# Performance work log

Measured on AMD Instinct MI355X. Metric: run time of the kernel, lower is better.

## Reference

```python
import jax, jax.numpy as jnp
import numpy as np

N_NODES = 10000
N_EDGES = 160000
IN_DIM = 512
HID = 256
HEADS = 4
OUT_DIM = 512
NEG_SLOPE = 0.2  # PyG GATConv default


def _glorot(key, shape):
    fan_in, fan_out = shape[0], shape[-1]
    lim = jnp.sqrt(6.0 / (fan_in + fan_out))
    return jax.random.uniform(key, shape, jnp.float32, -lim, lim)


def setup_inputs() -> dict:
    key = jax.random.key(0)
    ks = jax.random.split(key, 16)
    x = jax.random.normal(ks[0], (N_NODES, IN_DIM), jnp.float32)
    edge_index = jax.random.randint(ks[1], (2, N_EDGES), 0, N_NODES, jnp.int64)
    # layer 1: GATConv(512 -> 256, heads=4, concat) -> out 1024
    W1 = _glorot(ks[2], (IN_DIM, HEADS * HID))
    att_src1 = _glorot(ks[3], (HEADS, HID))
    att_dst1 = _glorot(ks[4], (HEADS, HID))
    b1 = jnp.zeros((HEADS * HID,), jnp.float32)
    # layer 2: GATConv(1024 -> 256, heads=4, concat) -> out 1024
    W2 = _glorot(ks[5], (HEADS * HID, HEADS * HID))
    att_src2 = _glorot(ks[6], (HEADS, HID))
    att_dst2 = _glorot(ks[7], (HEADS, HID))
    b2 = jnp.zeros((HEADS * HID,), jnp.float32)
    # final fc: 1024 -> 512
    fcW = _glorot(ks[8], (HEADS * HID, OUT_DIM))
    fcb = jnp.zeros((OUT_DIM,), jnp.float32)
    return dict(x=x, edge_index=edge_index, W1=W1, att_src1=att_src1,
                att_dst1=att_dst1, b1=b1, W2=W2, att_src2=att_src2,
                att_dst2=att_dst2, b2=b2, fcW=fcW, fcb=fcb)


def gat_conv(x, src, dst, W, att_src, att_dst, bias):
    # x: [N, F_in]; src/dst: [E] (self-loops already included)
    N = x.shape[0]
    h = (x @ W).reshape(N, HEADS, HID)                       # [N, H, C]
    a_src = jnp.sum(h * att_src, axis=-1)                    # [N, H]
    a_dst = jnp.sum(h * att_dst, axis=-1)                    # [N, H]
    e = jax.nn.leaky_relu(a_src[src] + a_dst[dst], NEG_SLOPE)  # [E, H]
    # numerically stable segment softmax over destination nodes
    m = jax.ops.segment_max(e, dst, num_segments=N)          # [N, H]
    e = jnp.exp(e - m[dst])
    s = jax.ops.segment_sum(e, dst, num_segments=N)          # [N, H]
    alpha = e / (s[dst] + 1e-16)                             # [E, H]
    msg = alpha[:, :, None] * h[src]                         # [E, H, C]
    out = jax.ops.segment_sum(msg, dst, num_segments=N)      # [N, H, C]
    return out.reshape(N, HEADS * HID) + bias


def reference(x, edge_index, W1, att_src1, att_dst1, b1,
              W2, att_src2, att_dst2, b2, fcW, fcb):
    N = x.shape[0]
    loops = jnp.arange(N, dtype=edge_index.dtype)
    src = jnp.concatenate([edge_index[0], loops])  # PyG add_self_loops=True
    dst = jnp.concatenate([edge_index[1], loops])
    h = gat_conv(x, src, dst, W1, att_src1, att_dst1, b1)
    h = jax.nn.relu(h)  # dropout is identity in eval mode
    h = gat_conv(h, src, dst, W2, att_src2, att_dst2, b2)
    h = jax.nn.relu(h)
    return h @ fcW + fcb
```

## Files before the change

kernel.cpp:

```cpp
#include <hip/hip_runtime.h>
#include <hip/hip_bf16.h>

#define NN 10000
#define NE 160000
#define NET 170000
#define IN_DIM 512
#define D1 1024
#define HEADS 4
#define HID 256
#define OUT_DIM 512
#define NEG_SLOPE 0.2f

typedef __attribute__((ext_vector_type(8))) short bf16x8;
typedef __attribute__((ext_vector_type(4))) float f32x4;

__device__ inline float b2f(unsigned short b) {
    union { unsigned u; float f; } x; x.u = ((unsigned)b) << 16; return x.f;
}
__device__ inline unsigned short f2b(float f) {
    union { float f; unsigned u; } x; x.f = f;
    unsigned u = x.u;
    unsigned r = u + 0x7FFFu + ((u >> 16) & 1u);
    return (unsigned short)(r >> 16);
}
__device__ inline float lrelu(float v) { return v > 0.f ? v : NEG_SLOPE * v; }

__device__ inline void load_edge(const void* ei, int f64, int e, int& s, int& d) {
    if (f64) {
        const long long* p = (const long long*)ei;
        s = (int)p[e]; d = (int)p[NE + e];
    } else {
        const int* p = (const int*)ei;
        s = p[e]; d = p[NE + e];
    }
}

__global__ void count_kernel(const void* ei, const int* flag, int* counts) {
    int e = blockIdx.x * blockDim.x + threadIdx.x;
    if (e >= NET) return;
    int s, d;
    if (e < NE) load_edge(ei, *flag, e, s, d);
    else d = e - NE;
    atomicAdd(&counts[d], 1);
}

__global__ __launch_bounds__(256) void scan_kernel(const int* counts, int* indptr) {
    __shared__ int part[256];
    int t = threadIdx.x;
    int base = t * 40;
    int local[40];
    int sum = 0;
#pragma unroll
    for (int k = 0; k < 40; k++) {
        int i = base + k;
        int c = (i < NN) ? counts[i] : 0;
        local[k] = sum;
        sum += c;
    }
    part[t] = sum;
    __syncthreads();
    for (int off = 1; off < 256; off <<= 1) {
        int v = (t >= off) ? part[t - off] : 0;
        __syncthreads();
        part[t] += v;
        __syncthreads();
    }
    int excl = part[t] - sum;
#pragma unroll
    for (int k = 0; k < 40; k++) {
        int i = base + k;
        if (i < NN) indptr[i] = excl + local[k];
    }
    if (t == 255) indptr[NN] = part[255];
}

__global__ void fill_kernel(const void* ei, const int* flag, const int* indptr,
                            int* cursor, int* csr_src) {
    int e = blockIdx.x * blockDim.x + threadIdx.x;
    if (e >= NET) return;
    int s, d;
    if (e < NE) load_edge(ei, *flag, e, s, d);
    else { s = e - NE; d = s; }
    int pos = indptr[d] + atomicAdd(&cursor[d], 1);
    csr_src[pos] = s;
}

__device__ void tpose_tile(const float* __restrict__ in, unsigned short* __restrict__ out,
                           int R, int C, int bx, int by) {
    __shared__ float tile[32][33];
    int tx = threadIdx.x & 31, ty = threadIdx.x >> 5;
    int c = bx * 32 + tx;
#pragma unroll
    for (int r0 = 0; r0 < 32; r0 += 8) {
        int r = by * 32 + ty + r0;
        tile[ty + r0][tx] = in[(size_t)r * C + c];
    }
    __syncthreads();
    int oc = by * 32 + tx;
#pragma unroll
    for (int r0 = 0; r0 < 32; r0 += 8) {
        int orow = bx * 32 + ty + r0;
        out[(size_t)orow * R + oc] = f2b(tile[tx][ty + r0]);
    }
}

#define INIT_NB 40
#define CVT_NB 5000
#define TP1_NB 512
#define TP2_NB 1024
#define TP3_NB 512
__global__ __launch_bounds__(256) void setup_kernel(
    const int* ei32, int* flag, int* counts, int* cursor,
    const float* __restrict__ x, unsigned short* __restrict__ xb,
    const float* __restrict__ W1, unsigned short* __restrict__ W1t,
    const float* __restrict__ W2, unsigned short* __restrict__ W2t,
    const float* __restrict__ fcW, unsigned short* __restrict__ fcWt) {
    int b = blockIdx.x;
    if (b < INIT_NB) {
        int i = b * 256 + threadIdx.x;
        if (i < NN) { counts[i] = 0; cursor[i] = 0; }
        if (b == 0) {
            __shared__ int nz;
            if (threadIdx.x == 0) nz = 0;
            __syncthreads();
            int acc = 0;
            for (int k = threadIdx.x; k < 500; k += 256) acc |= ei32[2 * k + 1];
            if (acc) atomicOr(&nz, 1);
            __syncthreads();
            if (threadIdx.x == 0) flag[0] = (nz == 0) ? 1 : 0;
        }
        return;
    }
    b -= INIT_NB;
    if (b < CVT_NB) {
        int i = b * 256 + threadIdx.x;
        float4 v = reinterpret_cast<const float4*>(x)[i];
        ushort4 o;
        o.x = f2b(v.x); o.y = f2b(v.y); o.z = f2b(v.z); o.w = f2b(v.w);
        reinterpret_cast<ushort4*>(xb)[i] = o;
        return;
    }
    b -= CVT_NB;
    if (b < TP1_NB) { tpose_tile(W1, W1t, IN_DIM, D1, b & 31, b >> 5); return; }
    b -= TP1_NB;
    if (b < TP2_NB) { tpose_tile(W2, W2t, D1, D1, b & 31, b >> 5); return; }
    b -= TP2_NB;
    tpose_tile(fcW, fcWt, D1, OUT_DIM, b & 15, b >> 4);
}

template<int TBM, int TBN>
__global__ __launch_bounds__(256) void gemmT(
    const unsigned short* __restrict__ A, const unsigned short* __restrict__ B,
    const float* __restrict__ bias, float* __restrict__ Cf, unsigned short* __restrict__ Cb,
    int M, int N, int K, int NB) {
    constexpr int FM = TBM / 32;
    constexpr int FN = TBN / 32;
    constexpr int AISS = TBM / 32;
    constexpr int BISS = TBN / 32;
    constexpr int ABUF = TBM * 64;
    constexpr int BBUF = TBN * 64;
    __shared__ __align__(16) unsigned short As[2 * ABUF];
    __shared__ __align__(16) unsigned short Bs[2 * BBUF];
    int t = threadIdx.x;
    int nwg = gridDim.x;
    int q = nwg >> 3, r = nwg & 7;
    int xcd = blockIdx.x & 7, jj = blockIdx.x >> 3;
    int wg = (xcd < r ? xcd * (q + 1) : r * (q + 1) + (xcd - r) * q) + jj;
    int row0 = (wg / NB) * TBM, col0 = (wg % NB) * TBN;

    int w = t >> 6, l = t & 63;
    int wr = w >> 1, wc = w & 1;
    f32x4 acc[FM][FN] = {};

    int srow = w * 8 + (l >> 3);
    int scs = ((l & 7) ^ (l >> 3)) * 8;
    const unsigned short* ap[AISS];
    const unsigned short* bp[BISS];
#pragma unroll
    for (int i = 0; i < AISS; i++)
        ap[i] = A + (size_t)min(row0 + i * 32 + srow, M - 1) * K + scs;
#pragma unroll
    for (int i = 0; i < BISS; i++)
        bp[i] = B + (size_t)(col0 + i * 32 + srow) * K + scs;

    int rr = l & 15;
    int rb = (rr & 7) << 4;
    int kb0 = (l >> 4) << 4;
    int c_l = l & 15, r_h = (l >> 4) * 4;

#define GLD(src, dst) __builtin_amdgcn_global_load_lds( \
        (const __attribute__((address_space(1))) void*)(src), \
        (__attribute__((address_space(3))) void*)(dst), 16, 0, 0)

#pragma unroll
    for (int i = 0; i < AISS; i++) { GLD(ap[i], As + i * 2048 + w * 512); ap[i] += 64; }
#pragma unroll
    for (int i = 0; i < BISS; i++) { GLD(bp[i], Bs + i * 2048 + w * 512); bp[i] += 64; }
    __syncthreads();

    int cur = 0;
    for (int k0 = 0; k0 < K; k0 += 64) {
        int nxt = cur ^ 1;
        if (k0 + 64 < K) {
#pragma unroll
            for (int i = 0; i < AISS; i++) {
                GLD(ap[i], As + nxt * ABUF + i * 2048 + w * 512);
                ap[i] += 64;
            }
#pragma unroll
            for (int i = 0; i < BISS; i++) {
                GLD(bp[i], Bs + nxt * BBUF + i * 2048 + w * 512);
                bp[i] += 64;
            }
        }
        const char* Ab = (const char*)(As + cur * ABUF);
        const char* Bb = (const char*)(Bs + cur * BBUF);
#pragma unroll
        for (int ks = 0; ks < 2; ks++) {
            int kb = ((ks << 6) | kb0) ^ rb;
            bf16x8 af[FM], bfv[FN];
#pragma unroll
            for (int mi = 0; mi < FM; mi++)
                af[mi] = *reinterpret_cast<const bf16x8*>(
                    Ab + (wr * (TBM / 2) + mi * 16 + rr) * 128 + kb);
#pragma unroll
            for (int ni = 0; ni < FN; ni++)
                bfv[ni] = *reinterpret_cast<const bf16x8*>(
                    Bb + (wc * (TBN / 2) + ni * 16 + rr) * 128 + kb);
#pragma unroll
            for (int mi = 0; mi < FM; mi++)
#pragma unroll
                for (int ni = 0; ni < FN; ni++)
                    acc[mi][ni] = __builtin_amdgcn_mfma_f32_16x16x32_bf16(
                        af[mi], bfv[ni], acc[mi][ni], 0, 0, 0);
        }
        __syncthreads();
        cur = nxt;
    }
#undef GLD

#pragma unroll
    for (int mi = 0; mi < FM; mi++)
#pragma unroll
        for (int ni = 0; ni < FN; ni++) {
            int gc = col0 + wc * (TBN / 2) + ni * 16 + c_l;
#pragma unroll
            for (int j = 0; j < 4; j++) {
                int gr = row0 + wr * (TBM / 2) + mi * 16 + r_h + j;
                if (gr < M) {
                    float v = acc[mi][ni][j];
                    if (bias) v += bias[gc];
                    if (Cf) Cf[(size_t)gr * N + gc] = v;
                    if (Cb) Cb[(size_t)gr * N + gc] = f2b(v);
                }
            }
        }
}

__global__ __launch_bounds__(256) void att_kernel(const unsigned short* __restrict__ hb,
                                                  const float* __restrict__ att_s,
                                                  const float* __restrict__ att_d,
                                                  float* __restrict__ aS, float* __restrict__ aD) {
    int node = blockIdx.x * 4 + (threadIdx.x >> 6);
    int l = threadIdx.x & 63;
    int head = l >> 4, qq = l & 15;
    const unsigned short* hrow = hb + (size_t)node * D1 + head * HID + qq * 16;
    bf16x8 h0 = *reinterpret_cast<const bf16x8*>(hrow);
    bf16x8 h1 = *reinterpret_cast<const bf16x8*>(hrow + 8);
    const float* asp = att_s + head * HID + qq * 16;
    const float* adp = att_d + head * HID + qq * 16;
    float ps = 0.f, pd = 0.f;
#pragma unroll
    for (int c = 0; c < 8; c++) {
        float hv = b2f((unsigned short)h0[c]);
        float hw = b2f((unsigned short)h1[c]);
        ps += hv * asp[c] + hw * asp[8 + c];
        pd += hv * adp[c] + hw * adp[8 + c];
    }
#pragma unroll
    for (int off = 1; off <= 8; off <<= 1) {
        ps += __shfl_xor(ps, off);
        pd += __shfl_xor(pd, off);
    }
    if (qq == 0) {
        aS[node * HEADS + head] = ps;
        aD[node * HEADS + head] = pd;
    }
}

__global__ __launch_bounds__(256) void agg_kernel(const unsigned short* __restrict__ hb,
                                                  const float* __restrict__ aS,
                                                  const float* __restrict__ aD,
                                                  const int* __restrict__ indptr,
                                                  const int* __restrict__ csr_src,
                                                  const float* __restrict__ bias,
                                                  unsigned short* __restrict__ outb) {
    int node = blockIdx.x * 4 + (threadIdx.x >> 6);
    int l = threadIdx.x & 63;
    int head = l >> 4;
    int beg = indptr[node];
    int deg = indptr[node + 1] - beg;
    float adst = aD[node * HEADS + head];
    const unsigned short* hp = hb + (size_t)l * 16;
    const int* cs = csr_src + beg;
    float acc[16];
#pragma unroll
    for (int c = 0; c < 16; c++) acc[c] = 0.f;
    float esum = 0.f;
    int dm = deg - 1;
    for (int j = 0; j < deg; j += 4) {
        int i0 = j, i1 = min(j + 1, dm), i2 = min(j + 2, dm), i3 = min(j + 3, dm);
        int s0 = cs[i0], s1 = cs[i1], s2 = cs[i2], s3 = cs[i3];
        const unsigned short* r0 = hp + (size_t)s0 * D1;
        const unsigned short* r1 = hp + (size_t)s1 * D1;
        const unsigned short* r2 = hp + (size_t)s2 * D1;
        const unsigned short* r3 = hp + (size_t)s3 * D1;
        bf16x8 r0a = *reinterpret_cast<const bf16x8*>(r0);
        bf16x8 r0b = *reinterpret_cast<const bf16x8*>(r0 + 8);
        bf16x8 r1a = *reinterpret_cast<const bf16x8*>(r1);
        bf16x8 r1b = *reinterpret_cast<const bf16x8*>(r1 + 8);
        bf16x8 r2a = *reinterpret_cast<const bf16x8*>(r2);
        bf16x8 r2b = *reinterpret_cast<const bf16x8*>(r2 + 8);
        bf16x8 r3a = *reinterpret_cast<const bf16x8*>(r3);
        bf16x8 r3b = *reinterpret_cast<const bf16x8*>(r3 + 8);
        float e0 = __expf(lrelu(aS[s0 * HEADS + head] + adst));
        float e1 = (j + 1 <= dm) ? __expf(lrelu(aS[s1 * HEADS + head] + adst)) : 0.f;
        float e2 = (j + 2 <= dm) ? __expf(lrelu(aS[s2 * HEADS + head] + adst)) : 0.f;
        float e3 = (j + 3 <= dm) ? __expf(lrelu(aS[s3 * HEADS + head] + adst)) : 0.f;
        esum += e0 + e1 + e2 + e3;
#pragma unroll
        for (int c = 0; c < 8; c++) {
            acc[c] += e0 * b2f((unsigned short)r0a[c]) + e1 * b2f((unsigned short)r1a[c])
                    + e2 * b2f((unsigned short)r2a[c]) + e3 * b2f((unsigned short)r3a[c]);
            acc[8 + c] += e0 * b2f((unsigned short)r0b[c]) + e1 * b2f((unsigned short)r1b[c])
                        + e2 * b2f((unsigned short)r2b[c]) + e3 * b2f((unsigned short)r3b[c]);
        }
    }
    float inv = 1.f / (esum + 1e-16f);
    const float* bp = bias + l * 16;
    bf16x8 o0, o1;
#pragma unroll
    for (int c = 0; c < 8; c++) {
        o0[c] = (short)f2b(fmaxf(acc[c] * inv + bp[c], 0.f));
        o1[c] = (short)f2b(fmaxf(acc[8 + c] * inv + bp[8 + c], 0.f));
    }
    unsigned short* op = outb + (size_t)node * D1 + l * 16;
    *reinterpret_cast<bf16x8*>(op) = o0;
    *reinterpret_cast<bf16x8*>(op + 8) = o1;
}

extern "C" void kernel_launch(void* const* d_in, const int* in_sizes, int n_in,
                              void* d_out, int out_size, void* d_ws, size_t ws_size,
                              hipStream_t stream) {
    const float* x   = (const float*)d_in[0];
    const void*  ei  = d_in[1];
    const float* W1  = (const float*)d_in[2];
    const float* as1 = (const float*)d_in[3];
    const float* ad1 = (const float*)d_in[4];
    const float* b1  = (const float*)d_in[5];
    const float* W2  = (const float*)d_in[6];
    const float* as2 = (const float*)d_in[7];
    const float* ad2 = (const float*)d_in[8];
    const float* b2  = (const float*)d_in[9];
    const float* fcW = (const float*)d_in[10];
    const float* fcb = (const float*)d_in[11];
    float* out = (float*)d_out;

    char* ws = (char*)d_ws;
    size_t o = 0;
    auto carve = [&](size_t bytes) -> char* {
        char* p = ws + o;
        o = (o + bytes + 255) & ~(size_t)255;
        return p;
    };
    unsigned short* xb   = (unsigned short*)carve((size_t)NN * IN_DIM * 2);
    unsigned short* hb   = (unsigned short*)carve((size_t)NN * D1 * 2);
    unsigned short* x2b  = (unsigned short*)carve((size_t)NN * D1 * 2);
    unsigned short* W1t  = (unsigned short*)carve((size_t)D1 * IN_DIM * 2);
    unsigned short* W2t  = (unsigned short*)carve((size_t)D1 * D1 * 2);
    unsigned short* fcWt = (unsigned short*)carve((size_t)OUT_DIM * D1 * 2);
    float* aS   = (float*)carve((size_t)NN * HEADS * 4);
    float* aD   = (float*)carve((size_t)NN * HEADS * 4);
    int* counts = (int*)carve((size_t)NN * 4);
    int* cursor = (int*)carve((size_t)NN * 4);
    int* indptr = (int*)carve((size_t)(NN + 1) * 4);
    int* csr_src= (int*)carve((size_t)NET * 4);
    int* flag   = (int*)carve(4);
    (void)ws_size; (void)in_sizes; (void)n_in; (void)out_size;

    setup_kernel<<<INIT_NB + CVT_NB + TP1_NB + TP2_NB + TP3_NB, 256, 0, stream>>>(
        (const int*)ei, flag, counts, cursor, x, xb, W1, W1t, W2, W2t, fcW, fcWt);
    count_kernel<<<(NET + 255) / 256, 256, 0, stream>>>(ei, flag, counts);
    scan_kernel<<<1, 256, 0, stream>>>(counts, indptr);
    fill_kernel<<<(NET + 255) / 256, 256, 0, stream>>>(ei, flag, indptr, cursor, csr_src);

    const int MB128 = (NN + 127) / 128;
    const int MB64  = (NN + 63) / 64;
    gemmT<128, 64><<<MB128 * (D1 / 64), 256, 0, stream>>>(xb, W1t, nullptr, nullptr, hb,
                                                          NN, D1, IN_DIM, D1 / 64);
    att_kernel<<<NN / 4, 256, 0, stream>>>(hb, as1, ad1, aS, aD);
    agg_kernel<<<NN / 4, 256, 0, stream>>>(hb, aS, aD, indptr, csr_src, b1, x2b);
    gemmT<128, 64><<<MB128 * (D1 / 64), 256, 0, stream>>>(x2b, W2t, nullptr, nullptr, hb,
                                                          NN, D1, D1, D1 / 64);
    att_kernel<<<NN / 4, 256, 0, stream>>>(hb, as2, ad2, aS, aD);
    agg_kernel<<<NN / 4, 256, 0, stream>>>(hb, aS, aD, indptr, csr_src, b2, x2b);
    gemmT<64, 64><<<MB64 * (OUT_DIM / 64), 256, 0, stream>>>(x2b, fcWt, fcb, out, nullptr,
                                                             NN, OUT_DIM, D1, OUT_DIM / 64);
}
```

Measured before the change: 239.9 us.

## Fold CSR build stages into setup, GEMM and attention kernels to cut launches

The separate count, scan and fill kernels are removed. Their work is appended as extra blocks: edge counting goes into the setup kernel, the prefix scan runs as one extra block of the first GEMM, and CSR fill runs as extra blocks of the first attention kernel. The int64 detection flag is replaced by a per-thread probe of 16 words, so the flag buffer is gone. This saves kernel launches and their serialization gaps, but the zero kernel now runs as its own launch and the lone scan block may lengthen the GEMM's tail.

After: 229.4 us, median of 2. -4.4%, faster.

```diff
diff --git a/kernel.cpp b/kernel.cpp
--- a/kernel.cpp
+++ b/kernel.cpp
@@ -25,7 +25,14 @@
 }
 __device__ inline float lrelu(float v) { return v > 0.f ? v : NEG_SLOPE * v; }
 
-__device__ inline void load_edge(const void* ei, int f64, int e, int& s, int& d) {
+__device__ inline bool is64(const int* ei32) {
+    int acc = 0;
+#pragma unroll
+    for (int k = 0; k < 16; k++) acc |= ei32[2 * k + 1];
+    return acc == 0;
+}
+
+__device__ inline void load_edge(const void* ei, bool f64, int e, int& s, int& d) {
     if (f64) {
         const long long* p = (const long long*)ei;
         s = (int)p[e]; d = (int)p[NE + e];
@@ -35,16 +42,12 @@
     }
 }
 
-__global__ void count_kernel(const void* ei, const int* flag, int* counts) {
-    int e = blockIdx.x * blockDim.x + threadIdx.x;
-    if (e >= NET) return;
-    int s, d;
-    if (e < NE) load_edge(ei, *flag, e, s, d);
-    else d = e - NE;
-    atomicAdd(&counts[d], 1);
-}
-
-__global__ __launch_bounds__(256) void scan_kernel(const int* counts, int* indptr) {
+__global__ void zero_kernel(int* counts, int* cursor) {
+    int i = blockIdx.x * blockDim.x + threadIdx.x;
+    if (i < NN) { counts[i] = 0; cursor[i] = 0; }
+}
+
+__device__ void scan_dev(const int* counts, int* indptr) {
     __shared__ int part[256];
     int t = threadIdx.x;
     int base = t * 40;
@@ -74,17 +77,6 @@
     if (t == 255) indptr[NN] = part[255];
 }
 
-__global__ void fill_kernel(const void* ei, const int* flag, const int* indptr,
-                            int* cursor, int* csr_src) {
-    int e = blockIdx.x * blockDim.x + threadIdx.x;
-    if (e >= NET) return;
-    int s, d;
-    if (e < NE) load_edge(ei, *flag, e, s, d);
-    else { s = e - NE; d = s; }
-    int pos = indptr[d] + atomicAdd(&cursor[d], 1);
-    csr_src[pos] = s;
-}
-
 __device__ void tpose_tile(const float* __restrict__ in, unsigned short* __restrict__ out,
                            int R, int C, int bx, int by) {
     __shared__ float tile[32][33];
@@ -104,34 +96,18 @@
     }
 }
 
-#define INIT_NB 40
 #define CVT_NB 5000
 #define TP1_NB 512
 #define TP2_NB 1024
 #define TP3_NB 512
+#define CNT_NB 665
 __global__ __launch_bounds__(256) void setup_kernel(
-    const int* ei32, int* flag, int* counts, int* cursor,
+    const void* ei, int* counts,
     const float* __restrict__ x, unsigned short* __restrict__ xb,
     const float* __restrict__ W1, unsigned short* __restrict__ W1t,
     const float* __restrict__ W2, unsigned short* __restrict__ W2t,
     const float* __restrict__ fcW, unsigned short* __restrict__ fcWt) {
     int b = blockIdx.x;
-    if (b < INIT_NB) {
-        int i = b * 256 + threadIdx.x;
-        if (i < NN) { counts[i] = 0; cursor[i] = 0; }
-        if (b == 0) {
-            __shared__ int nz;
-            if (threadIdx.x == 0) nz = 0;
-            __syncthreads();
-            int acc = 0;
-            for (int k = threadIdx.x; k < 500; k += 256) acc |= ei32[2 * k + 1];
-            if (acc) atomicOr(&nz, 1);
-            __syncthreads();
-            if (threadIdx.x == 0) flag[0] = (nz == 0) ? 1 : 0;
-        }
-        return;
-    }
-    b -= INIT_NB;
     if (b < CVT_NB) {
         int i = b * 256 + threadIdx.x;
         float4 v = reinterpret_cast<const float4*>(x)[i];
@@ -145,14 +121,24 @@
     b -= TP1_NB;
     if (b < TP2_NB) { tpose_tile(W2, W2t, D1, D1, b & 31, b >> 5); return; }
     b -= TP2_NB;
-    tpose_tile(fcW, fcWt, D1, OUT_DIM, b & 15, b >> 4);
+    if (b < TP3_NB) { tpose_tile(fcW, fcWt, D1, OUT_DIM, b & 15, b >> 4); return; }
+    b -= TP3_NB;
+    int e = b * 256 + threadIdx.x;
+    if (e >= NET) return;
+    bool f64 = is64((const int*)ei);
+    int s, d;
+    if (e < NE) load_edge(ei, f64, e, s, d);
+    else d = e - NE;
+    atomicAdd(&counts[d], 1);
 }
 
 template<int TBM, int TBN>
 __global__ __launch_bounds__(256) void gemmT(
     const unsigned short* __restrict__ A, const unsigned short* __restrict__ B,
     const float* __restrict__ bias, float* __restrict__ Cf, unsigned short* __restrict__ Cb,
-    int M, int N, int K, int NB) {
+    int M, int N, int K, int NB, int NWG,
+    const int* __restrict__ sc_counts, int* __restrict__ sc_indptr) {
+    if ((int)blockIdx.x >= NWG) { scan_dev(sc_counts, sc_indptr); return; }
     constexpr int FM = TBM / 32;
     constexpr int FN = TBN / 32;
     constexpr int AISS = TBM / 32;
@@ -162,8 +148,7 @@
     __shared__ __align__(16) unsigned short As[2 * ABUF];
     __shared__ __align__(16) unsigned short Bs[2 * BBUF];
     int t = threadIdx.x;
-    int nwg = gridDim.x;
-    int q = nwg >> 3, r = nwg & 7;
+    int q = NWG >> 3, r = NWG & 7;
     int xcd = blockIdx.x & 7, jj = blockIdx.x >> 3;
     int wg = (xcd < r ? xcd * (q + 1) : r * (q + 1) + (xcd - r) * q) + jj;
     int row0 = (wg / NB) * TBM, col0 = (wg % NB) * TBN;
@@ -257,10 +242,23 @@
         }
 }
 
-__global__ __launch_bounds__(256) void att_kernel(const unsigned short* __restrict__ hb,
-                                                  const float* __restrict__ att_s,
-                                                  const float* __restrict__ att_d,
-                                                  float* __restrict__ aS, float* __restrict__ aD) {
+__global__ __launch_bounds__(256) void att_fill_kernel(
+    const unsigned short* __restrict__ hb,
+    const float* __restrict__ att_s, const float* __restrict__ att_d,
+    float* __restrict__ aS, float* __restrict__ aD,
+    const void* ei, const int* __restrict__ indptr,
+    int* __restrict__ cursor, int* __restrict__ csr_src, int NATT) {
+    if ((int)blockIdx.x >= NATT) {
+        int e = ((int)blockIdx.x - NATT) * 256 + threadIdx.x;
+        if (e >= NET) return;
+        bool f64 = is64((const int*)ei);
+        int s, d;
+        if (e < NE) load_edge(ei, f64, e, s, d);
+        else { s = e - NE; d = s; }
+        int pos = indptr[d] + atomicAdd(&cursor[d], 1);
+        csr_src[pos] = s;
+        return;
+    }
     int node = blockIdx.x * 4 + (threadIdx.x >> 6);
     int l = threadIdx.x & 63;
     int head = l >> 4, qq = l & 15;
@@ -385,25 +383,30 @@
     int* cursor = (int*)carve((size_t)NN * 4);
     int* indptr = (int*)carve((size_t)(NN + 1) * 4);
     int* csr_src= (int*)carve((size_t)NET * 4);
-    int* flag   = (int*)carve(4);
     (void)ws_size; (void)in_sizes; (void)n_in; (void)out_size;
-
-    setup_kernel<<<INIT_NB + CVT_NB + TP1_NB + TP2_NB + TP3_NB, 256, 0, stream>>>(
-        (const int*)ei, flag, counts, cursor, x, xb, W1, W1t, W2, W2t, fcW, fcWt);
-    count_kernel<<<(NET + 255) / 256, 256, 0, stream>>>(ei, flag, counts);
-    scan_kernel<<<1, 256, 0, stream>>>(counts, indptr);
-    fill_kernel<<<(NET + 255) / 256, 256, 0, stream>>>(ei, flag, indptr, cursor, csr_src);
 
     const int MB128 = (NN + 127) / 128;
     const int MB64  = (NN + 63) / 64;
-    gemmT<128, 64><<<MB128 * (D1 / 64), 256, 0, stream>>>(xb, W1t, nullptr, nullptr, hb,
-                                                          NN, D1, IN_DIM, D1 / 64);
-    att_kernel<<<NN / 4, 256, 0, stream>>>(hb, as1, ad1, aS, aD);
-    agg_kernel<<<NN / 4, 256, 0, stream>>>(hb, aS, aD, indptr, csr_src, b1, x2b);
-    gemmT<128, 64><<<MB128 * (D1 / 64), 256, 0, stream>>>(x2b, W2t, nullptr, nullptr, hb,
-                                                          NN, D1, D1, D1 / 64);
-    att_kernel<<<NN / 4, 256, 0, stream>>>(hb, as2, ad2, aS, aD);
-    agg_kernel<<<NN / 4, 256, 0, stream>>>(hb, aS, aD, indptr, csr_src, b2, x2b);
-    gemmT<64, 64><<<MB64 * (OUT_DIM / 64), 256, 0, stream>>>(x2b, fcWt, fcb, out, nullptr,
-                                                             NN, OUT_DIM, D1, OUT_DIM / 64);
-}
+    const int G1 = MB128 * (D1 / 64);
+    const int GF = MB64 * (OUT_DIM / 64);
+    const int NATT = NN / 4;
+
+    zero_kernel<<<(NN + 255) / 256, 256, 0, stream>>>(counts, cursor);
+    setup_kernel<<<CVT_NB + TP1_NB + TP2_NB + TP3_NB + CNT_NB, 256, 0, stream>>>(
+        ei, counts, x, xb, W1, W1t, W2, W2t, fcW, fcWt);
+    gemmT<128, 64><<<G1 + 1, 256, 0, stream>>>(xb, W1t, nullptr, nullptr, hb,
+                                               NN, D1, IN_DIM, D1 / 64, G1,
+                                               counts, indptr);
+    att_fill_kernel<<<NATT + CNT_NB, 256, 0, stream>>>(hb, as1, ad1, aS, aD,
+                                                       ei, indptr, cursor, csr_src, NATT);
+    agg_kernel<<<NATT, 256, 0, stream>>>(hb, aS, aD, indptr, csr_src, b1, x2b);
+    gemmT<128, 64><<<G1, 256, 0, stream>>>(x2b, W2t, nullptr, nullptr, hb,
+                                           NN, D1, D1, D1 / 64, G1,
+                                           nullptr, nullptr);
+    att_fill_kernel<<<NATT, 256, 0, stream>>>(hb, as2, ad2, aS, aD,
+                                              ei, indptr, cursor, csr_src, NATT);
+    agg_kernel<<<NATT, 256, 0, stream>>>(hb, aS, aD, indptr, csr_src, b2, x2b);
+    gemmT<64, 64><<<GF, 256, 0, stream>>>(x2b, fcWt, fcb, out, nullptr,
+                                          NN, OUT_DIM, D1, OUT_DIM / 64, GF,
+                                          nullptr, nullptr);
+}
```
